# Kernel tuning notes

Hardware: AMD Instinct MI355X
Metric: run time of the kernel (lower is better)

## Reference

```python
import jax, jax.numpy as jnp
import numpy as np

N_NODES = 50000
IN_CH, HID, OUT_CH = 512, 128, 64
N_EDGES = 800000


def gcn_conv(x, edge_index, W, b, num_nodes):
    # PyG GCNConv: add self-loops, symmetric deg^{-1/2} normalization,
    # linear transform then scatter-add aggregation at target nodes.
    row, col = edge_index[0], edge_index[1]
    loop = jnp.arange(num_nodes, dtype=row.dtype)
    rows = jnp.concatenate([row, loop])  # sources
    cols = jnp.concatenate([col, loop])  # targets
    deg = jax.ops.segment_sum(jnp.ones_like(cols, dtype=x.dtype), cols, num_segments=num_nodes)
    dinv = jnp.where(deg > 0, jax.lax.rsqrt(deg), 0.0)
    norm = dinv[rows] * dinv[cols]  # [E+N]
    h = x @ W  # [N, out]
    msg = norm[:, None] * h[rows]  # gather + scale
    out = jax.ops.segment_sum(msg, cols, num_segments=num_nodes)
    return out + b


def setup_inputs() -> dict:
    key = jax.random.key(0)
    k = jax.random.split(key, 8)
    x = jax.random.normal(k[0], (N_NODES, IN_CH), dtype=jnp.float32)
    pos_edge_index = jax.random.randint(k[1], (2, N_EDGES), 0, N_NODES, dtype=jnp.int64 if jax.config.jax_enable_x64 else jnp.int32)
    neg_edge_index = jax.random.randint(k[2], (2, N_EDGES), 0, N_NODES, dtype=pos_edge_index.dtype)
    # Glorot-ish init for weights, zeros for bias (PyG default)
    W1 = jax.random.normal(k[3], (IN_CH, HID), dtype=jnp.float32) * (1.0 / np.sqrt(IN_CH))
    b1 = jnp.zeros((HID,), dtype=jnp.float32)
    W2 = jax.random.normal(k[4], (HID, OUT_CH), dtype=jnp.float32) * (1.0 / np.sqrt(HID))
    b2 = jnp.zeros((OUT_CH,), dtype=jnp.float32)
    return {"x": x, "pos_edge_index": pos_edge_index, "neg_edge_index": neg_edge_index,
            "W1": W1, "b1": b1, "W2": W2, "b2": b2}


def reference(x, pos_edge_index, neg_edge_index, W1, b1, W2, b2):
    n = x.shape[0]
    h = gcn_conv(x, pos_edge_index, W1, b1, n)
    h = jax.nn.relu(h)
    z = gcn_conv(h, pos_edge_index, W2, b2, n)  # encode
    edge_index = jnp.concatenate([pos_edge_index, neg_edge_index], axis=-1)
    # decode: per-edge dot product of endpoint embeddings
    logits = jnp.sum(z[edge_index[0]] * z[edge_index[1]], axis=-1)
    return logits
```

## Files before the change

### kernel.cpp

```cpp
#include <hip/hip_runtime.h>

#define WAVE 64
#define CAP 64
#define CURPAD 16

typedef __bf16 v8bf __attribute__((ext_vector_type(8)));
typedef __bf16 v4bf __attribute__((ext_vector_type(4)));
typedef __bf16 v2bf __attribute__((ext_vector_type(2)));
typedef float f32x4 __attribute__((ext_vector_type(4)));

__device__ __forceinline__ void async16(void* lds, const void* g) {
    __builtin_amdgcn_global_load_lds((const __attribute__((address_space(1))) void*)g,
                                     (__attribute__((address_space(3))) void*)lds, 16, 0, 0);
}

__device__ __forceinline__ void cvt8(const f32x4& u, const f32x4& v, v8bf& h, v8bf& l) {
    float f[8] = {u.x, u.y, u.z, u.w, v.x, v.y, v.z, v.w};
#pragma unroll
    for (int j = 0; j < 8; ++j) {
        __bf16 hh = (__bf16)f[j];
        h[j] = hh;
        l[j] = (__bf16)(f[j] - (float)hh);
    }
}

__device__ __forceinline__ void cvt8f(const float4& u, const float4& v, v8bf& h, v8bf& l) {
    float f[8] = {u.x, u.y, u.z, u.w, v.x, v.y, v.z, v.w};
#pragma unroll
    for (int j = 0; j < 8; ++j) {
        __bf16 hh = (__bf16)f[j];
        h[j] = hh;
        l[j] = (__bf16)(f[j] - (float)hh);
    }
}

__global__ __launch_bounds__(256) void prep_kernel(const float* __restrict__ W1,
                                                   const float* __restrict__ W2,
                                                   __bf16* __restrict__ Wt1hi,
                                                   __bf16* __restrict__ Wt1lo,
                                                   __bf16* __restrict__ Wt2hi,
                                                   __bf16* __restrict__ Wt2lo) {
    int b = blockIdx.x;
    int tid = threadIdx.x;
    if (b < 256) {
        int idx = b * 256 + tid;
        int k = idx >> 7, n = idx & 127;
        float v = W1[idx];
        __bf16 h = (__bf16)v;
        Wt1hi[n * 512 + k] = h;
        Wt1lo[n * 512 + k] = (__bf16)(v - (float)h);
    } else {
        int idx = (b - 256) * 256 + tid;
        int k = idx >> 6, n = idx & 63;
        float v = W2[idx];
        __bf16 h = (__bf16)v;
        int o = (k >> 5) * (64 * 32) + n * 32 + (k & 31);
        Wt2hi[o] = h;
        Wt2lo[o] = (__bf16)(v - (float)h);
    }
}

template <int NC, int KK, bool OBF16>
__global__ __launch_bounds__(256, 3) void gemm_fill_kernel(
    const float* __restrict__ A, const __bf16* __restrict__ Bhi,
    const __bf16* __restrict__ Blo, void* __restrict__ Cout, int M, int NG,
    const int* __restrict__ ei, int E, int* __restrict__ cursor,
    unsigned short* __restrict__ srcs) {
    constexpr int BK = 32;
    constexpr int NT = NC / 16;
    constexpr int NIT = KK / BK;
    constexpr int NCH = NC / 16;

    __shared__ __bf16 sB[2][2][NC * BK];

    const int tid = threadIdx.x;

    if (blockIdx.x >= NG) {
        int bb = (blockIdx.x - NG) * 512;
#pragma unroll
        for (int j = 0; j < 2; ++j) {
            int e = bb + tid + j * 256;
            if (e < E) {
                int dst = ei[E + e];
                int p = atomicAdd(&cursor[(size_t)dst * CURPAD], 1);
                if (p < CAP) srcs[(size_t)dst * CAP + p] = (unsigned short)ei[e];
            }
        }
        return;
    }

    const int lane = tid & 63;
    const int wv = tid >> 6;
    const int ln15 = lane & 15;
    const int quad = lane >> 4;
    const int rowBase = blockIdx.x * 128;

    const int brow = lane >> 2;
    const int bslot = lane & 3;
    auto stageB = [&](int buf, int k0) {
#pragma unroll
        for (int i = 0; i < NCH / 4; ++i) {
            int c = wv * (NCH / 4) + i;
            int row = c * 16 + brow;
            int gk = k0 + ((bslot ^ (row & 3)) << 3);
            async16(&sB[buf][0][c * 512], Bhi + (size_t)row * KK + gk);
            async16(&sB[buf][1][c * 512], Blo + (size_t)row * KK + gk);
        }
    };

    int r0 = rowBase + wv * 32 + ln15;
    int r1 = r0 + 16;
    if (r0 > M - 1) r0 = M - 1;
    if (r1 > M - 1) r1 = M - 1;
    const float* aP0 = A + (size_t)r0 * KK + quad * 8;
    const float* aP1 = A + (size_t)r1 * KK + quad * 8;

    f32x4 acc[2][NT];
#pragma unroll
    for (int rt = 0; rt < 2; ++rt)
#pragma unroll
        for (int t = 0; t < NT; ++t) acc[rt][t] = (f32x4){0.f, 0.f, 0.f, 0.f};

    float4 aR[4];
    aR[0] = *(const float4*)(aP0);
    aR[1] = *(const float4*)(aP0 + 4);
    aR[2] = *(const float4*)(aP1);
    aR[3] = *(const float4*)(aP1 + 4);

    stageB(0, 0);
    __syncthreads();

    int cur = 0;
    for (int ks = 0; ks < NIT; ++ks) {
        if (ks + 1 < NIT) stageB(cur ^ 1, (ks + 1) * BK);

        v8bf ah[2], al[2];
        cvt8f(aR[0], aR[1], ah[0], al[0]);
        cvt8f(aR[2], aR[3], ah[1], al[1]);
        if (ks + 1 < NIT) {
            aP0 += BK;
            aP1 += BK;
            aR[0] = *(const float4*)(aP0);
            aR[1] = *(const float4*)(aP0 + 4);
            aR[2] = *(const float4*)(aP1);
            aR[3] = *(const float4*)(aP1 + 4);
        }

#pragma unroll
        for (int t = 0; t < NT; ++t) {
            int row = t * 16 + ln15;
            int off = row * BK + ((quad ^ (row & 3)) << 3);
            v8bf bh = *(const v8bf*)&sB[cur][0][off];
            v8bf bl = *(const v8bf*)&sB[cur][1][off];
            acc[0][t] = __builtin_amdgcn_mfma_f32_16x16x32_bf16(ah[0], bh, acc[0][t], 0, 0, 0);
            acc[0][t] = __builtin_amdgcn_mfma_f32_16x16x32_bf16(al[0], bh, acc[0][t], 0, 0, 0);
            acc[0][t] = __builtin_amdgcn_mfma_f32_16x16x32_bf16(ah[0], bl, acc[0][t], 0, 0, 0);
            acc[1][t] = __builtin_amdgcn_mfma_f32_16x16x32_bf16(ah[1], bh, acc[1][t], 0, 0, 0);
            acc[1][t] = __builtin_amdgcn_mfma_f32_16x16x32_bf16(al[1], bh, acc[1][t], 0, 0, 0);
            acc[1][t] = __builtin_amdgcn_mfma_f32_16x16x32_bf16(ah[1], bl, acc[1][t], 0, 0, 0);
        }

        __syncthreads();
        cur ^= 1;
    }

#pragma unroll
    for (int rt = 0; rt < 2; ++rt) {
#pragma unroll
        for (int r = 0; r < 4; ++r) {
            int grow = rowBase + wv * 32 + rt * 16 + quad * 4 + r;
            if (grow < M) {
#pragma unroll
                for (int t = 0; t < NT; ++t) {
                    float v = acc[rt][t][r];
                    if (OBF16)
                        ((__bf16*)Cout)[(size_t)grow * NC + t * 16 + ln15] = (__bf16)v;
                    else
                        ((float*)Cout)[(size_t)grow * NC + t * 16 + ln15] = v;
                }
            }
        }
    }
}

__global__ __launch_bounds__(256) void dinv_kernel(const int* __restrict__ cursor,
                                                   float* __restrict__ dinv, int N) {
    int i = blockIdx.x * 256 + (int)threadIdx.x;
    if (i < N) dinv[i] = rsqrtf((float)cursor[(size_t)i * CURPAD] + 1.0f);
}

__global__ __launch_bounds__(256) void gather1_gemm2_kernel(
    const __bf16* __restrict__ hs, const int* __restrict__ counts,
    const float* __restrict__ dinv, const unsigned short* __restrict__ srcs,
    const float* __restrict__ bias, const __bf16* __restrict__ W2hi,
    const __bf16* __restrict__ W2lo, __bf16* __restrict__ hs2, int N) {
    constexpr int LDO = 132;
    __shared__ float out1[16 * LDO];

    const int tid = threadIdx.x;
    const int lane = tid & 63;
    const int wv = tid >> 6;
    const int base = blockIdx.x * 16;

    for (int i = 0; i < 4; ++i) {
        int slot = wv * 4 + i;
        int node = base + slot;
        float v0 = 0.f, v1 = 0.f;
        int col = 2 * lane;
        if (node < N) {
            int cnt = counts[(size_t)node * CURPAD];
            if (cnt > CAP) cnt = CAP;
            int beg = node * CAP;
            int end = beg + cnt;
            float dn = rsqrtf((float)cnt + 1.0f);
            float a0, a1;
            {
                v2bf s = *(const v2bf*)&hs[(size_t)node * 128 + col];
                a0 = dn * (float)s[0];
                a1 = dn * (float)s[1];
            }
            int e = beg;
            for (; e + 8 <= end; e += 8) {
                int s0 = srcs[e], s1 = srcs[e + 1], s2 = srcs[e + 2], s3 = srcs[e + 3];
                int s4 = srcs[e + 4], s5 = srcs[e + 5], s6 = srcs[e + 6], s7 = srcs[e + 7];
                float d0 = dinv[s0], d1 = dinv[s1], d2 = dinv[s2], d3 = dinv[s3];
                float d4 = dinv[s4], d5 = dinv[s5], d6 = dinv[s6], d7 = dinv[s7];
                v2bf r0 = *(const v2bf*)&hs[(size_t)s0 * 128 + col];
                v2bf r1 = *(const v2bf*)&hs[(size_t)s1 * 128 + col];
                v2bf r2 = *(const v2bf*)&hs[(size_t)s2 * 128 + col];
                v2bf r3 = *(const v2bf*)&hs[(size_t)s3 * 128 + col];
                v2bf r4 = *(const v2bf*)&hs[(size_t)s4 * 128 + col];
                v2bf r5 = *(const v2bf*)&hs[(size_t)s5 * 128 + col];
                v2bf r6 = *(const v2bf*)&hs[(size_t)s6 * 128 + col];
                v2bf r7 = *(const v2bf*)&hs[(size_t)s7 * 128 + col];
                a0 += d0 * (float)r0[0] + d1 * (float)r1[0] + d2 * (float)r2[0] + d3 * (float)r3[0] +
                      d4 * (float)r4[0] + d5 * (float)r5[0] + d6 * (float)r6[0] + d7 * (float)r7[0];
                a1 += d0 * (float)r0[1] + d1 * (float)r1[1] + d2 * (float)r2[1] + d3 * (float)r3[1] +
                      d4 * (float)r4[1] + d5 * (float)r5[1] + d6 * (float)r6[1] + d7 * (float)r7[1];
            }
            for (; e < end; ++e) {
                int s0 = srcs[e];
                float d0 = dinv[s0];
                v2bf r0 = *(const v2bf*)&hs[(size_t)s0 * 128 + col];
                a0 += d0 * (float)r0[0];
                a1 += d0 * (float)r0[1];
            }
            float2 bv = *(const float2*)&bias[col];
            v0 = fmaxf(dn * a0 + bv.x, 0.f);
            v1 = fmaxf(dn * a1 + bv.y, 0.f);
        }
        *(float2*)&out1[slot * LDO + col] = make_float2(v0, v1);
    }
    __syncthreads();

    const int ln15 = lane & 15;
    const int quad = lane >> 4;
    f32x4 acc = (f32x4){0.f, 0.f, 0.f, 0.f};
#pragma unroll
    for (int kc = 0; kc < 4; ++kc) {
        const float* ap = &out1[ln15 * LDO + kc * 32 + quad * 8];
        f32x4 u = *(const f32x4*)(ap);
        f32x4 v = *(const f32x4*)(ap + 4);
        v8bf ah, al;
        cvt8(u, v, ah, al);
        size_t bo = (size_t)kc * (64 * 32) + (wv * 16 + ln15) * 32 + quad * 8;
        v8bf bh = *(const v8bf*)(W2hi + bo);
        v8bf bl = *(const v8bf*)(W2lo + bo);
        acc = __builtin_amdgcn_mfma_f32_16x16x32_bf16(ah, bh, acc, 0, 0, 0);
        acc = __builtin_amdgcn_mfma_f32_16x16x32_bf16(al, bh, acc, 0, 0, 0);
        acc = __builtin_amdgcn_mfma_f32_16x16x32_bf16(ah, bl, acc, 0, 0, 0);
    }
#pragma unroll
    for (int r = 0; r < 4; ++r) {
        int node = base + quad * 4 + r;
        if (node < N) hs2[(size_t)node * 64 + wv * 16 + ln15] = (__bf16)acc[r];
    }
}

__global__ __launch_bounds__(256) void gather_agg2(const __bf16* __restrict__ hs,
                                                   const int* __restrict__ counts,
                                                   const float* __restrict__ dinv,
                                                   const unsigned short* __restrict__ srcs,
                                                   const float* __restrict__ bias,
                                                   __bf16* __restrict__ outp, int N) {
    int node = blockIdx.x * 4 + (int)(threadIdx.x >> 6);
    if (node >= N) return;
    int lane = threadIdx.x & 63;
    int cnt = counts[(size_t)node * CURPAD];
    if (cnt > CAP) cnt = CAP;
    int beg = node * CAP;
    int end = beg + cnt;
    float dn = rsqrtf((float)cnt + 1.0f);

    int q = lane >> 4;
    int sl = lane & 15;
    int col = sl * 4;
    float a0 = 0.f, a1 = 0.f, a2 = 0.f, a3 = 0.f;
    if (q == 0) {
        v4bf s = *(const v4bf*)&hs[(size_t)node * 64 + col];
        a0 = dn * (float)s[0]; a1 = dn * (float)s[1];
        a2 = dn * (float)s[2]; a3 = dn * (float)s[3];
    }
    int e = beg + q;
    for (; e + 12 < end; e += 16) {
        int s0 = srcs[e], s1 = srcs[e + 4], s2 = srcs[e + 8], s3 = srcs[e + 12];
        float d0 = dinv[s0], d1 = dinv[s1], d2 = dinv[s2], d3 = dinv[s3];
        v4bf r0 = *(const v4bf*)&hs[(size_t)s0 * 64 + col];
        v4bf r1 = *(const v4bf*)&hs[(size_t)s1 * 64 + col];
        v4bf r2 = *(const v4bf*)&hs[(size_t)s2 * 64 + col];
        v4bf r3 = *(const v4bf*)&hs[(size_t)s3 * 64 + col];
        a0 += d0 * (float)r0[0] + d1 * (float)r1[0] + d2 * (float)r2[0] + d3 * (float)r3[0];
        a1 += d0 * (float)r0[1] + d1 * (float)r1[1] + d2 * (float)r2[1] + d3 * (float)r3[1];
        a2 += d0 * (float)r0[2] + d1 * (float)r1[2] + d2 * (float)r2[2] + d3 * (float)r3[2];
        a3 += d0 * (float)r0[3] + d1 * (float)r1[3] + d2 * (float)r2[3] + d3 * (float)r3[3];
    }
    for (; e < end; e += 4) {
        int s0 = srcs[e];
        float d0 = dinv[s0];
        v4bf r0 = *(const v4bf*)&hs[(size_t)s0 * 64 + col];
        a0 += d0 * (float)r0[0]; a1 += d0 * (float)r0[1];
        a2 += d0 * (float)r0[2]; a3 += d0 * (float)r0[3];
    }
    a0 += __shfl_xor(a0, 16); a0 += __shfl_xor(a0, 32);
    a1 += __shfl_xor(a1, 16); a1 += __shfl_xor(a1, 32);
    a2 += __shfl_xor(a2, 16); a2 += __shfl_xor(a2, 32);
    a3 += __shfl_xor(a3, 16); a3 += __shfl_xor(a3, 32);
    if (q == 0) {
        float4 bv = *(const float4*)&bias[col];
        v4bf o;
        o[0] = (__bf16)(dn * a0 + bv.x);
        o[1] = (__bf16)(dn * a1 + bv.y);
        o[2] = (__bf16)(dn * a2 + bv.z);
        o[3] = (__bf16)(dn * a3 + bv.w);
        *(v4bf*)&outp[(size_t)node * 64 + col] = o;
    }
}

__global__ __launch_bounds__(256) void decode_bf16_kernel(const __bf16* __restrict__ z,
                                                          const int* __restrict__ pos,
                                                          const int* __restrict__ neg, int E,
                                                          float* __restrict__ out) {
    int tid = blockIdx.x * blockDim.x + threadIdx.x;
    int g = tid >> 2;
    int l = tid & 3;
    int total = 2 * E;
    if (g >= total) return;
    int src, dst;
    if (g < E) {
        src = pos[g];
        dst = pos[E + g];
    } else {
        int e = g - E;
        src = neg[e];
        dst = neg[E + e];
    }
    const __bf16* zs = z + (size_t)src * 64 + l * 16;
    const __bf16* zd = z + (size_t)dst * 64 + l * 16;
    v8bf a0 = *(const v8bf*)zs;
    v8bf a1 = *(const v8bf*)(zs + 8);
    v8bf b0 = *(const v8bf*)zd;
    v8bf b1 = *(const v8bf*)(zd + 8);
    float p = 0.f;
#pragma unroll
    for (int j = 0; j < 8; ++j) p += (float)a0[j] * (float)b0[j] + (float)a1[j] * (float)b1[j];
    p += __shfl_xor(p, 1);
    p += __shfl_xor(p, 2);
    if (l == 0) out[g] = p;
}

extern "C" void kernel_launch(void* const* d_in, const int* in_sizes, int n_in, void* d_out,
                              int out_size, void* d_ws, size_t ws_size, hipStream_t stream) {
    const float* x = (const float*)d_in[0];
    const int* pos_ei = (const int*)d_in[1];
    const int* neg_ei = (const int*)d_in[2];
    const float* W1 = (const float*)d_in[3];
    const float* b1 = (const float*)d_in[4];
    const float* W2 = (const float*)d_in[5];
    const float* b2 = (const float*)d_in[6];
    float* out = (float*)d_out;

    const int IN = 512, HID = 128, OUT = 64;
    const int N = in_sizes[0] / IN;
    const int E = in_sizes[1] / 2;

    size_t nAlign = ((size_t)N + 255) & ~(size_t)255;
    float* p = (float*)d_ws;
    __bf16* hs1 = (__bf16*)p; p += (size_t)N * HID / 2;
    __bf16* hs2 = (__bf16*)p; p += (size_t)N * OUT / 2;
    __bf16* zbf = (__bf16*)p; p += (size_t)N * OUT / 2;
    int* cursor = (int*)p; p += nAlign * CURPAD;
    float* dinv = p; p += nAlign;
    unsigned short* srcs = (unsigned short*)p; p += (size_t)N * CAP / 2;
    __bf16* Wt1hi = (__bf16*)p; p += (size_t)IN * HID / 2;
    __bf16* Wt1lo = (__bf16*)p; p += (size_t)IN * HID / 2;
    __bf16* Wt2hi = (__bf16*)p; p += (size_t)HID * OUT / 2;
    __bf16* Wt2lo = (__bf16*)p; p += (size_t)HID * OUT / 2;

    const int NG = (N + 127) / 128;
    const int NF = (E + 511) / 512;

    hipMemsetAsync(cursor, 0, (size_t)N * CURPAD * sizeof(int), stream);
    prep_kernel<<<288, 256, 0, stream>>>(W1, W2, Wt1hi, Wt1lo, Wt2hi, Wt2lo);

    gemm_fill_kernel<128, 512, true><<<NG + NF, 256, 0, stream>>>(
        x, Wt1hi, Wt1lo, hs1, N, NG, pos_ei, E, cursor, srcs);

    dinv_kernel<<<(N + 255) / 256, 256, 0, stream>>>(cursor, dinv, N);

    gather1_gemm2_kernel<<<(N + 15) / 16, 256, 0, stream>>>(
        hs1, cursor, dinv, srcs, b1, Wt2hi, Wt2lo, hs2, N);

    gather_agg2<<<(N + 3) / 4, 256, 0, stream>>>(hs2, cursor, dinv, srcs, b2, zbf, N);

    decode_bf16_kernel<<<((size_t)2 * E * 4 + 255) / 256, 256, 0, stream>>>(
        zbf, pos_ei, neg_ei, E, out);
}
```

Measured before the change: 315.5 us.

## Split layer-2 features into two 32-column planes for gather and decode

```diff
diff --git a/kernel.cpp b/kernel.cpp
--- a/kernel.cpp
+++ b/kernel.cpp
@@ -270,19 +270,21 @@
         acc = __builtin_amdgcn_mfma_f32_16x16x32_bf16(al, bh, acc, 0, 0, 0);
         acc = __builtin_amdgcn_mfma_f32_16x16x32_bf16(ah, bl, acc, 0, 0, 0);
     }
+    const size_t pbase = (size_t)(wv >> 1) * ((size_t)N * 32);
+    const int icol = (wv & 1) * 16 + ln15;
 #pragma unroll
     for (int r = 0; r < 4; ++r) {
         int node = base + quad * 4 + r;
-        if (node < N) hs2[(size_t)node * 64 + wv * 16 + ln15] = (__bf16)acc[r];
-    }
-}
-
-__global__ __launch_bounds__(256) void gather_agg2(const __bf16* __restrict__ hs,
-                                                   const int* __restrict__ counts,
-                                                   const float* __restrict__ dinv,
-                                                   const unsigned short* __restrict__ srcs,
-                                                   const float* __restrict__ bias,
-                                                   __bf16* __restrict__ outp, int N) {
+        if (node < N) hs2[pbase + (size_t)node * 32 + icol] = (__bf16)acc[r];
+    }
+}
+
+__global__ __launch_bounds__(256) void gather2_plane(const __bf16* __restrict__ hp,
+                                                     const int* __restrict__ counts,
+                                                     const float* __restrict__ dinv,
+                                                     const unsigned short* __restrict__ srcs,
+                                                     const float* __restrict__ biasp,
+                                                     __bf16* __restrict__ zp, int N) {
     int node = blockIdx.x * 4 + (int)(threadIdx.x >> 6);
     if (node >= N) return;
     int lane = threadIdx.x & 63;
@@ -294,68 +296,63 @@
 
     int q = lane >> 4;
     int sl = lane & 15;
-    int col = sl * 4;
-    float a0 = 0.f, a1 = 0.f, a2 = 0.f, a3 = 0.f;
+    int col = sl * 2;
+    float a0 = 0.f, a1 = 0.f;
     if (q == 0) {
-        v4bf s = *(const v4bf*)&hs[(size_t)node * 64 + col];
-        a0 = dn * (float)s[0]; a1 = dn * (float)s[1];
-        a2 = dn * (float)s[2]; a3 = dn * (float)s[3];
+        v2bf s = *(const v2bf*)&hp[(size_t)node * 32 + col];
+        a0 = dn * (float)s[0];
+        a1 = dn * (float)s[1];
     }
     int e = beg + q;
     for (; e + 12 < end; e += 16) {
         int s0 = srcs[e], s1 = srcs[e + 4], s2 = srcs[e + 8], s3 = srcs[e + 12];
         float d0 = dinv[s0], d1 = dinv[s1], d2 = dinv[s2], d3 = dinv[s3];
-        v4bf r0 = *(const v4bf*)&hs[(size_t)s0 * 64 + col];
-        v4bf r1 = *(const v4bf*)&hs[(size_t)s1 * 64 + col];
-        v4bf r2 = *(const v4bf*)&hs[(size_t)s2 * 64 + col];
-        v4bf r3 = *(const v4bf*)&hs[(size_t)s3 * 64 + col];
+        v2bf r0 = *(const v2bf*)&hp[(size_t)s0 * 32 + col];
+        v2bf r1 = *(const v2bf*)&hp[(size_t)s1 * 32 + col];
+        v2bf r2 = *(const v2bf*)&hp[(size_t)s2 * 32 + col];
+        v2bf r3 = *(const v2bf*)&hp[(size_t)s3 * 32 + col];
         a0 += d0 * (float)r0[0] + d1 * (float)r1[0] + d2 * (float)r2[0] + d3 * (float)r3[0];
         a1 += d0 * (float)r0[1] + d1 * (float)r1[1] + d2 * (float)r2[1] + d3 * (float)r3[1];
-        a2 += d0 * (float)r0[2] + d1 * (float)r1[2] + d2 * (float)r2[2] + d3 * (float)r3[2];
-        a3 += d0 * (float)r0[3] + d1 * (float)r1[3] + d2 * (float)r2[3] + d3 * (float)r3[3];
     }
     for (; e < end; e += 4) {
         int s0 = srcs[e];
         float d0 = dinv[s0];
-        v4bf r0 = *(const v4bf*)&hs[(size_t)s0 * 64 + col];
-        a0 += d0 * (float)r0[0]; a1 += d0 * (float)r0[1];
-        a2 += d0 * (float)r0[2]; a3 += d0 * (float)r0[3];
+        v2bf r0 = *(const v2bf*)&hp[(size_t)s0 * 32 + col];
+        a0 += d0 * (float)r0[0];
+        a1 += d0 * (float)r0[1];
     }
     a0 += __shfl_xor(a0, 16); a0 += __shfl_xor(a0, 32);
     a1 += __shfl_xor(a1, 16); a1 += __shfl_xor(a1, 32);
-    a2 += __shfl_xor(a2, 16); a2 += __shfl_xor(a2, 32);
-    a3 += __shfl_xor(a3, 16); a3 += __shfl_xor(a3, 32);
     if (q == 0) {
-        float4 bv = *(const float4*)&bias[col];
-        v4bf o;
+        float2 bv = *(const float2*)&biasp[col];
+        v2bf o;
         o[0] = (__bf16)(dn * a0 + bv.x);
         o[1] = (__bf16)(dn * a1 + bv.y);
-        o[2] = (__bf16)(dn * a2 + bv.z);
-        o[3] = (__bf16)(dn * a3 + bv.w);
-        *(v4bf*)&outp[(size_t)node * 64 + col] = o;
-    }
-}
-
-__global__ __launch_bounds__(256) void decode_bf16_kernel(const __bf16* __restrict__ z,
-                                                          const int* __restrict__ pos,
-                                                          const int* __restrict__ neg, int E,
-                                                          float* __restrict__ out) {
+        *(v2bf*)&zp[(size_t)node * 32 + col] = o;
+    }
+}
+
+template <bool ADD>
+__global__ __launch_bounds__(256) void decode_plane(const __bf16* __restrict__ zp,
+                                                    const int* __restrict__ pos,
+                                                    const int* __restrict__ neg, int E,
+                                                    float* __restrict__ out) {
     int tid = blockIdx.x * blockDim.x + threadIdx.x;
-    int g = tid >> 2;
-    int l = tid & 3;
+    int g = tid >> 1;
+    int l = tid & 1;
     int total = 2 * E;
     if (g >= total) return;
     int src, dst;
     if (g < E) {
-        src = pos[g];
-        dst = pos[E + g];
+        src = __builtin_nontemporal_load(&pos[g]);
+        dst = __builtin_nontemporal_load(&pos[E + g]);
     } else {
         int e = g - E;
-        src = neg[e];
-        dst = neg[E + e];
-    }
-    const __bf16* zs = z + (size_t)src * 64 + l * 16;
-    const __bf16* zd = z + (size_t)dst * 64 + l * 16;
+        src = __builtin_nontemporal_load(&neg[e]);
+        dst = __builtin_nontemporal_load(&neg[E + e]);
+    }
+    const __bf16* zs = zp + (size_t)src * 32 + l * 16;
+    const __bf16* zd = zp + (size_t)dst * 32 + l * 16;
     v8bf a0 = *(const v8bf*)zs;
     v8bf a1 = *(const v8bf*)(zs + 8);
     v8bf b0 = *(const v8bf*)zd;
@@ -364,8 +361,14 @@
 #pragma unroll
     for (int j = 0; j < 8; ++j) p += (float)a0[j] * (float)b0[j] + (float)a1[j] * (float)b1[j];
     p += __shfl_xor(p, 1);
-    p += __shfl_xor(p, 2);
-    if (l == 0) out[g] = p;
+    if (l == 0) {
+        if (ADD) {
+            float prev = __builtin_nontemporal_load(&out[g]);
+            __builtin_nontemporal_store(prev + p, &out[g]);
+        } else {
+            __builtin_nontemporal_store(p, &out[g]);
+        }
+    }
 }
 
 extern "C" void kernel_launch(void* const* d_in, const int* in_sizes, int n_in, void* d_out,
@@ -396,6 +399,8 @@
     __bf16* Wt2hi = (__bf16*)p; p += (size_t)HID * OUT / 2;
     __bf16* Wt2lo = (__bf16*)p; p += (size_t)HID * OUT / 2;
 
+    const size_t PL = (size_t)N * 32;
+
     const int NG = (N + 127) / 128;
     const int NF = (E + 511) / 512;
 
@@ -410,8 +415,11 @@
     gather1_gemm2_kernel<<<(N + 15) / 16, 256, 0, stream>>>(
         hs1, cursor, dinv, srcs, b1, Wt2hi, Wt2lo, hs2, N);
 
-    gather_agg2<<<(N + 3) / 4, 256, 0, stream>>>(hs2, cursor, dinv, srcs, b2, zbf, N);
-
-    decode_bf16_kernel<<<((size_t)2 * E * 4 + 255) / 256, 256, 0, stream>>>(
-        zbf, pos_ei, neg_ei, E, out);
-}
+    gather2_plane<<<(N + 3) / 4, 256, 0, stream>>>(hs2, cursor, dinv, srcs, b2, zbf, N);
+    gather2_plane<<<(N + 3) / 4, 256, 0, stream>>>(hs2 + PL, cursor, dinv, srcs, b2 + 32,
+                                                   zbf + PL, N);
+
+    const int NDEC = (int)(((size_t)2 * E * 2 + 255) / 256);
+    decode_plane<false><<<NDEC, 256, 0, stream>>>(zbf, pos_ei, neg_ei, E, out);
+    decode_plane<true><<<NDEC, 256, 0, stream>>>(zbf + PL, pos_ei, neg_ei, E, out);
+}
```

Measured after the change: 351.7 us. +11.5%, slower.
